# Performance work log

Hardware: AMD Instinct MI355X
Metric: run time of the kernel (lower is better)

Reference implementation:

```python
import jax, jax.numpy as jnp
import numpy as np

S, B, N, DIM = 64, 4, 256, 256
HEADS, DIM_HEAD = 8, 32
INNER = HEADS * DIM_HEAD  # 256
SCALE = DIM_HEAD ** -0.5
NEG = -1e10


def setup_inputs() -> dict:
    key = jax.random.key(0)
    k1, k2, k3, k4, k5 = jax.random.split(key, 5)
    x = jax.random.normal(k1, (S, B, N, DIM), dtype=jnp.float32)
    mask = jax.random.randint(k2, (S, N, N), 0, 2, dtype=jnp.int32)
    # nn.Linear(dim, inner*3, bias=False): y = x @ W_qkv  (W stored transposed)
    W_qkv = jax.random.normal(k3, (DIM, 3 * INNER), dtype=jnp.float32) / np.sqrt(DIM)
    W_out = jax.random.normal(k4, (INNER, DIM), dtype=jnp.float32) / np.sqrt(INNER)
    b_out = jax.random.normal(k5, (DIM,), dtype=jnp.float32) * 0.01
    return {"x": x, "mask": mask, "W_qkv": W_qkv, "W_out": W_out, "b_out": b_out}


def reference(x, mask, W_qkv, W_out, b_out):
    s, b, n, _ = x.shape
    qkv = x @ W_qkv                                  # [s,b,n,3*inner]
    q, k, v = jnp.split(qkv, 3, axis=-1)
    def to_heads(t):
        # s b n (h d) -> s b h n d
        return t.reshape(s, b, n, HEADS, DIM_HEAD).transpose(0, 1, 3, 2, 4)
    q, k, v = to_heads(q), to_heads(k), to_heads(v)
    sim = jnp.einsum('sbhid,sbhjd->sbhij', q, k) * SCALE
    sim = jnp.where(mask[:, None, None, :, :] == 0, NEG, sim)
    attn = jax.nn.softmax(sim, axis=-1)
    out = jnp.einsum('sbhij,sbhjd->sbhid', attn, v)
    out = out.transpose(0, 1, 3, 2, 4).reshape(s, b, n, INNER)  # s b h n d -> s b n (h d)
    return out @ W_out + b_out
```

## Files before the change

kernel.cpp:

```cpp
#include <hip/hip_runtime.h>

typedef __attribute__((ext_vector_type(8))) short bf16x8;
typedef __attribute__((ext_vector_type(4))) float f32x4;

__device__ __forceinline__ unsigned short f2bf(float f) {
  unsigned int u = __builtin_bit_cast(unsigned int, f);
  u += 0x7fffu + ((u >> 16) & 1u);
  return (unsigned short)(u >> 16);
}

typedef const __attribute__((address_space(1))) unsigned int* as1_u32p;
typedef __attribute__((address_space(3))) unsigned int* as3_u32p;
__device__ __forceinline__ void glds16(const void* g, void* l) {
  __builtin_amdgcn_global_load_lds((as1_u32p)g, (as3_u32p)l, 16, 0, 0);
}

__global__ __launch_bounds__(256) void cvt_kernel(const float* __restrict__ X,
                                                  unsigned short* __restrict__ Y) {
  const long long i = ((long long)blockIdx.x * 256 + threadIdx.x) * 8;
  float4 a = *reinterpret_cast<const float4*>(X + i);
  float4 b = *reinterpret_cast<const float4*>(X + i + 4);
  bf16x8 t;
  t[0] = (short)f2bf(a.x); t[1] = (short)f2bf(a.y);
  t[2] = (short)f2bf(a.z); t[3] = (short)f2bf(a.w);
  t[4] = (short)f2bf(b.x); t[5] = (short)f2bf(b.y);
  t[6] = (short)f2bf(b.z); t[7] = (short)f2bf(b.w);
  *reinterpret_cast<bf16x8*>(Y + i) = t;
}

__global__ __launch_bounds__(256) void transpose_bf16_kernel(
    const float* __restrict__ S, unsigned short* __restrict__ D, int R, int C) {
  __shared__ float T[32][33];
  const int bx = blockIdx.x * 32;
  const int by = blockIdx.y * 32;
  const int tx = threadIdx.x & 31, ty = threadIdx.x >> 5;
#pragma unroll
  for (int k = 0; k < 4; ++k)
    T[ty + 8 * k][tx] = S[(size_t)(by + ty + 8 * k) * C + bx + tx];
  __syncthreads();
#pragma unroll
  for (int k = 0; k < 4; ++k)
    D[(size_t)(bx + ty + 8 * k) * R + by + tx] = f2bf(T[tx][ty + 8 * k]);
}

template <bool C_F32>
__global__ __launch_bounds__(256) void gemm_bt(
    const unsigned short* __restrict__ A,
    const unsigned short* __restrict__ Bt,
    void* __restrict__ Cv,
    const float* __restrict__ bias,
    int M, int N, int K)
{
  __shared__ __align__(16) unsigned short As[128 * 32];
  __shared__ __align__(16) unsigned short Bs[128 * 32];

  const int tid  = threadIdx.x;
  const int bm   = blockIdx.x * 128;
  const int bn   = blockIdx.y * 128;
  const int lane = tid & 63;
  const int wave = tid >> 6;
  const int wr   = (wave >> 1) * 64;
  const int wc   = (wave & 1) * 64;
  const int l15  = lane & 15;
  const int quad = lane >> 4;

  f32x4 acc[4][4];
#pragma unroll
  for (int r = 0; r < 4; ++r)
#pragma unroll
    for (int c = 0; c < 4; ++c) {
      f32x4 z = {0.f, 0.f, 0.f, 0.f};
      acc[r][c] = z;
    }

  const unsigned short* gA0 = A  + (size_t)(bm + wave * 16 + (lane >> 2)) * K + (lane & 3) * 8;
  const unsigned short* gA1 = gA0 + (size_t)64 * K;
  const unsigned short* gB0 = Bt + (size_t)(bn + wave * 16 + (lane >> 2)) * K + (lane & 3) * 8;
  const unsigned short* gB1 = gB0 + (size_t)64 * K;
  unsigned short* lA0 = As + wave * 512;
  unsigned short* lA1 = As + 2048 + wave * 512;
  unsigned short* lB0 = Bs + wave * 512;
  unsigned short* lB1 = Bs + 2048 + wave * 512;

  for (int kk = 0; kk < K; kk += 32) {
    glds16(gA0 + kk, lA0);
    glds16(gA1 + kk, lA1);
    glds16(gB0 + kk, lB0);
    glds16(gB1 + kk, lB1);
    __syncthreads();

    bf16x8 af[4], bf[4];
#pragma unroll
    for (int i = 0; i < 4; ++i) {
      af[i] = *reinterpret_cast<const bf16x8*>(&As[(wr + i * 16 + l15) * 32 + quad * 8]);
      bf[i] = *reinterpret_cast<const bf16x8*>(&Bs[(wc + i * 16 + l15) * 32 + quad * 8]);
    }
#pragma unroll
    for (int rt = 0; rt < 4; ++rt)
#pragma unroll
      for (int ct = 0; ct < 4; ++ct)
        acc[rt][ct] = __builtin_amdgcn_mfma_f32_16x16x32_bf16(af[rt], bf[ct], acc[rt][ct], 0, 0, 0);
    __syncthreads();
  }

#pragma unroll
  for (int rt = 0; rt < 4; ++rt)
#pragma unroll
    for (int ct = 0; ct < 4; ++ct)
#pragma unroll
      for (int i = 0; i < 4; ++i) {
        const int row = bm + wr + rt * 16 + quad * 4 + i;
        const int col = bn + wc + ct * 16 + l15;
        const float v = acc[rt][ct][i];
        if constexpr (C_F32) {
          ((float*)Cv)[(size_t)row * N + col] = v + bias[col];
        } else {
          ((unsigned short*)Cv)[(size_t)row * N + col] = f2bf(v);
        }
      }
}

#define SCALE_F 0.17677669529663689f

__global__ __launch_bounds__(256) void attn_kernel(
    const unsigned short* __restrict__ QKV,
    const int* __restrict__ mask,
    unsigned short* __restrict__ Aout)
{
  __shared__ __align__(16) unsigned short Ks[256 * 40];
  __shared__ __align__(16) unsigned short SH[4 * 16 * 280];

  const int blk  = blockIdx.x;
  const int h    = blk & 7;
  const int sb   = blk >> 3;
  const int s    = sb >> 2;
  const int t0   = sb << 8;
  const int tid  = threadIdx.x;
  const int lane = tid & 63;
  const int wave = tid >> 6;
  const int l15  = lane & 15;
  const int quad = lane >> 4;

  {
    const unsigned short* kp = QKV + (size_t)(t0 + tid) * 768 + 256 + h * 32;
    const unsigned short* vp = kp + 256;
    unsigned short* kd = Ks + tid * 40;
    unsigned short* vd = SH + tid * 40;
#pragma unroll
    for (int i = 0; i < 4; ++i) {
      *reinterpret_cast<uint4*>(kd + i * 8) = *reinterpret_cast<const uint4*>(kp + i * 8);
      *reinterpret_cast<uint4*>(vd + i * 8) = *reinterpret_cast<const uint4*>(vp + i * 8);
    }
  }
  __syncthreads();

  bf16x8 bv[2][8];
#pragma unroll
  for (int dt = 0; dt < 2; ++dt)
#pragma unroll
    for (int ks = 0; ks < 8; ++ks) {
      bf16x8 v;
#pragma unroll
      for (int j = 0; j < 8; ++j)
        v[j] = (short)SH[(ks * 32 + quad * 8 + j) * 40 + dt * 16 + l15];
      bv[dt][ks] = v;
    }
  __syncthreads();

  unsigned short* P = SH + wave * (16 * 280);

  for (int qb = 0; qb < 4; ++qb) {
    const int qbase = wave * 64 + qb * 16;

    bf16x8 qf = *reinterpret_cast<const bf16x8*>(
        QKV + (size_t)(t0 + qbase + l15) * 768 + h * 32 + quad * 8);

    f32x4 sim[16];
#pragma unroll
    for (int ct = 0; ct < 16; ++ct) {
      bf16x8 kf = *reinterpret_cast<const bf16x8*>(&Ks[(ct * 16 + l15) * 40 + quad * 8]);
      f32x4 z = {0.f, 0.f, 0.f, 0.f};
      sim[ct] = __builtin_amdgcn_mfma_f32_16x16x32_bf16(qf, kf, z, 0, 0, 0);
    }

    float lsum[4];
#pragma unroll
    for (int i = 0; i < 4; ++i) {
      const int qrow = qbase + quad * 4 + i;
      const int* mrow = mask + ((size_t)s * 256 + qrow) * 256 + l15;
      float mx = -3.0e38f;
#pragma unroll
      for (int ct = 0; ct < 16; ++ct) {
        float v = sim[ct][i] * SCALE_F;
        if (mrow[ct * 16] == 0) v = -1.0e10f;
        sim[ct][i] = v;
        mx = fmaxf(mx, v);
      }
#pragma unroll
      for (int off = 1; off < 16; off <<= 1)
        mx = fmaxf(mx, __shfl_xor(mx, off, 64));
      float sum = 0.f;
#pragma unroll
      for (int ct = 0; ct < 16; ++ct) {
        float e = __expf(sim[ct][i] - mx);
        sim[ct][i] = e;
        sum += e;
      }
#pragma unroll
      for (int off = 1; off < 16; off <<= 1)
        sum += __shfl_xor(sum, off, 64);
      lsum[i] = sum;
    }

#pragma unroll
    for (int i = 0; i < 4; ++i)
#pragma unroll
      for (int ct = 0; ct < 16; ++ct)
        P[(quad * 4 + i) * 280 + ct * 16 + l15] = f2bf(sim[ct][i]);
    __syncthreads();

    f32x4 o0 = {0.f, 0.f, 0.f, 0.f};
    f32x4 o1 = {0.f, 0.f, 0.f, 0.f};
#pragma unroll
    for (int ks = 0; ks < 8; ++ks) {
      bf16x8 pf = *reinterpret_cast<const bf16x8*>(&P[l15 * 280 + ks * 32 + quad * 8]);
      o0 = __builtin_amdgcn_mfma_f32_16x16x32_bf16(pf, bv[0][ks], o0, 0, 0, 0);
      o1 = __builtin_amdgcn_mfma_f32_16x16x32_bf16(pf, bv[1][ks], o1, 0, 0, 0);
    }

#pragma unroll
    for (int i = 0; i < 4; ++i) {
      const float rl = 1.0f / lsum[i];
      const size_t row = (size_t)t0 + qbase + quad * 4 + i;
      Aout[row * 256 + h * 32 + l15]      = f2bf(o0[i] * rl);
      Aout[row * 256 + h * 32 + 16 + l15] = f2bf(o1[i] * rl);
    }
    __syncthreads();
  }
}

extern "C" void kernel_launch(void* const* d_in, const int* in_sizes, int n_in,
                              void* d_out, int out_size, void* d_ws, size_t ws_size,
                              hipStream_t stream) {
  const float* X    = (const float*)d_in[0];
  const int*   mask = (const int*)d_in[1];
  const float* Wqkv = (const float*)d_in[2];
  const float* Wout = (const float*)d_in[3];
  const float* bout = (const float*)d_in[4];
  float*       outp = (float*)d_out;

  unsigned short* QKV   = (unsigned short*)d_ws;
  unsigned short* Xbf   = QKV + (size_t)65536 * 768;
  unsigned short* Amid  = Xbf;
  unsigned short* WoutT = QKV;
  unsigned short* WqkvT = (unsigned short*)d_out;

  dim3 blk(256);
  cvt_kernel<<<dim3(8192), blk, 0, stream>>>(X, Xbf);
  transpose_bf16_kernel<<<dim3(24, 8), blk, 0, stream>>>(Wqkv, WqkvT, 256, 768);

  gemm_bt<false><<<dim3(512, 6), blk, 0, stream>>>(Xbf, WqkvT, (void*)QKV, nullptr, 65536, 768, 256);
  attn_kernel<<<dim3(2048), blk, 0, stream>>>(QKV, mask, Amid);

  transpose_bf16_kernel<<<dim3(8, 8), blk, 0, stream>>>(Wout, WoutT, 256, 256);
  gemm_bt<true><<<dim3(512, 2), blk, 0, stream>>>(Amid, WoutT, (void*)outp, bout, 65536, 256, 256);
}
```

Baseline: 320.2 us.

## Pack attention mask into bitfields and swizzle K/V shared-memory layout

Adds a pre-pass that packs the int32 mask into 16-bit bitfields per row/lane, so each attention block reads the mask once per head instead of re-reading 4-byte ints for all 8 heads. The attention kernel then tests mask bits from registers. It also replaces K's padded shared layout with an XOR swizzle and changes V's row stride to 38 with 4-byte stores to cut bank conflicts. This costs an extra kernel launch and a scratch buffer placed inside the output tensor, which is overwritten later.

```diff
diff --git a/kernel.cpp b/kernel.cpp
--- a/kernel.cpp
+++ b/kernel.cpp
@@ -43,6 +43,19 @@
     D[(size_t)(bx + ty + 8 * k) * R + by + tx] = f2bf(T[tx][ty + 8 * k]);
 }
 
+__global__ __launch_bounds__(256) void pack_mask_kernel(const int* __restrict__ mask,
+                                                        unsigned short* __restrict__ Mb) {
+  const int t = blockIdx.x * 256 + threadIdx.x;
+  const int l = t & 15;
+  const int r = t >> 4;
+  const int* mp = mask + ((size_t)r << 8) + l;
+  unsigned int bits = 0;
+#pragma unroll
+  for (int ct = 0; ct < 16; ++ct)
+    bits |= (mp[ct << 4] != 0 ? (1u << ct) : 0u);
+  Mb[t] = (unsigned short)bits;
+}
+
 template <bool C_F32>
 __global__ __launch_bounds__(256) void gemm_bt(
     const unsigned short* __restrict__ A,
@@ -124,10 +137,10 @@
 
 __global__ __launch_bounds__(256) void attn_kernel(
     const unsigned short* __restrict__ QKV,
-    const int* __restrict__ mask,
+    const unsigned short* __restrict__ Mb,
     unsigned short* __restrict__ Aout)
 {
-  __shared__ __align__(16) unsigned short Ks[256 * 40];
+  __shared__ __align__(16) unsigned short Ks[256 * 32];
   __shared__ __align__(16) unsigned short SH[4 * 16 * 280];
 
   const int blk  = blockIdx.x;
@@ -144,13 +157,15 @@
   {
     const unsigned short* kp = QKV + (size_t)(t0 + tid) * 768 + 256 + h * 32;
     const unsigned short* vp = kp + 256;
-    unsigned short* kd = Ks + tid * 40;
-    unsigned short* vd = SH + tid * 40;
-#pragma unroll
-    for (int i = 0; i < 4; ++i) {
-      *reinterpret_cast<uint4*>(kd + i * 8) = *reinterpret_cast<const uint4*>(kp + i * 8);
-      *reinterpret_cast<uint4*>(vd + i * 8) = *reinterpret_cast<const uint4*>(vp + i * 8);
-    }
+    const int sw = (tid >> 1) & 3;
+    unsigned short* kd = Ks + tid * 32;
+    unsigned short* vd = SH + tid * 38;
+#pragma unroll
+    for (int g = 0; g < 4; ++g)
+      *reinterpret_cast<uint4*>(kd + ((g ^ sw) << 3)) = *reinterpret_cast<const uint4*>(kp + g * 8);
+#pragma unroll
+    for (int i = 0; i < 16; ++i)
+      *reinterpret_cast<unsigned int*>(vd + i * 2) = *reinterpret_cast<const unsigned int*>(vp + i * 2);
   }
   __syncthreads();
 
@@ -162,12 +177,13 @@
       bf16x8 v;
 #pragma unroll
       for (int j = 0; j < 8; ++j)
-        v[j] = (short)SH[(ks * 32 + quad * 8 + j) * 40 + dt * 16 + l15];
+        v[j] = (short)SH[(ks * 32 + quad * 8 + j) * 38 + dt * 16 + l15];
       bv[dt][ks] = v;
     }
   __syncthreads();
 
   unsigned short* P = SH + wave * (16 * 280);
+  const int swr = (l15 >> 1) & 3;
 
   for (int qb = 0; qb < 4; ++qb) {
     const int qbase = wave * 64 + qb * 16;
@@ -175,10 +191,16 @@
     bf16x8 qf = *reinterpret_cast<const bf16x8*>(
         QKV + (size_t)(t0 + qbase + l15) * 768 + h * 32 + quad * 8);
 
+    unsigned short mbits[4];
+#pragma unroll
+    for (int i = 0; i < 4; ++i)
+      mbits[i] = Mb[(((size_t)s << 12)) + ((size_t)(qbase + quad * 4 + i) << 4) + l15];
+
     f32x4 sim[16];
 #pragma unroll
     for (int ct = 0; ct < 16; ++ct) {
-      bf16x8 kf = *reinterpret_cast<const bf16x8*>(&Ks[(ct * 16 + l15) * 40 + quad * 8]);
+      bf16x8 kf = *reinterpret_cast<const bf16x8*>(
+          &Ks[(ct * 16 + l15) * 32 + ((quad ^ swr) << 3)]);
       f32x4 z = {0.f, 0.f, 0.f, 0.f};
       sim[ct] = __builtin_amdgcn_mfma_f32_16x16x32_bf16(qf, kf, z, 0, 0, 0);
     }
@@ -186,13 +208,12 @@
     float lsum[4];
 #pragma unroll
     for (int i = 0; i < 4; ++i) {
-      const int qrow = qbase + quad * 4 + i;
-      const int* mrow = mask + ((size_t)s * 256 + qrow) * 256 + l15;
+      const unsigned int mw = mbits[i];
       float mx = -3.0e38f;
 #pragma unroll
       for (int ct = 0; ct < 16; ++ct) {
         float v = sim[ct][i] * SCALE_F;
-        if (mrow[ct * 16] == 0) v = -1.0e10f;
+        if (!((mw >> ct) & 1u)) v = -1.0e10f;
         sim[ct][i] = v;
         mx = fmaxf(mx, v);
       }
@@ -254,13 +275,15 @@
   unsigned short* Amid  = Xbf;
   unsigned short* WoutT = QKV;
   unsigned short* WqkvT = (unsigned short*)d_out;
+  unsigned short* Mbits = (unsigned short*)d_out + ((size_t)16 << 20);
 
   dim3 blk(256);
   cvt_kernel<<<dim3(8192), blk, 0, stream>>>(X, Xbf);
   transpose_bf16_kernel<<<dim3(24, 8), blk, 0, stream>>>(Wqkv, WqkvT, 256, 768);
+  pack_mask_kernel<<<dim3(1024), blk, 0, stream>>>(mask, Mbits);
 
   gemm_bt<false><<<dim3(512, 6), blk, 0, stream>>>(Xbf, WqkvT, (void*)QKV, nullptr, 65536, 768, 256);
-  attn_kernel<<<dim3(2048), blk, 0, stream>>>(QKV, mask, Amid);
+  attn_kernel<<<dim3(2048), blk, 0, stream>>>(QKV, Mbits, Amid);
 
   transpose_bf16_kernel<<<dim3(8, 8), blk, 0, stream>>>(Wout, WoutT, 256, 256);
   gemm_bt<true><<<dim3(512, 2), blk, 0, stream>>>(Amid, WoutT, (void*)outp, bout, 65536, 256, 256);
```

Measured after the change: 301.1 us. 6.0% less time.
